# Kernel tuning notes

Measured on AMD Instinct MI355X. Metric: run time of the kernel, lower is better.

## Reference

```python
import jax, jax.numpy as jnp
import numpy as np

N_A, N_F, N_K = 512, 128, 20


def setup_inputs() -> dict:
    key = jax.random.key(0)
    ks = jax.random.split(key, 12)
    b1 = (6.0 / N_K) ** 0.5   # uniform bound for w1/w2 weights
    s_phi = 0.5 * (6.0 / N_F) ** 0.5
    inp = {
        "x": jax.random.normal(ks[0], (1, N_A, N_F), jnp.float32),
        "e": jax.random.uniform(ks[1], (1, N_A, N_A - 1, N_K), jnp.float32),
        "mask": (jax.random.uniform(ks[2], (1, N_A, N_A - 1, 1)) > 0.1).astype(jnp.float32),
        "loop_mask": ~jnp.eye(N_A, dtype=bool)[None],  # (1, n_a, n_a), False on diagonal
        "w1_w": jax.random.uniform(ks[3], (N_F, N_K), jnp.float32, -b1, b1),
        "w1_b": jnp.zeros((N_F,), jnp.float32),
        "w2_w": jax.random.uniform(ks[4], (N_F, N_K), jnp.float32, -b1, b1),
        "w2_b": jnp.zeros((N_F,), jnp.float32),
        "phi_w": s_phi * jax.random.normal(ks[5], (N_F, N_F), jnp.float32),
        "phi_b": jnp.zeros((N_F,), jnp.float32),
        "o_w": 0.05 * jax.random.normal(ks[6], (3 * N_F, 2 * N_F), jnp.float32),
        "o_b": jnp.zeros((3 * N_F,), jnp.float32),
    }
    return inp


def reference(x, e, mask, loop_mask, w1_w, w1_b, w2_w, w2_b, phi_w, phi_b, o_w, o_b):
    silu = jax.nn.silu
    # filter-generating networks on RBF expansion e: (1, n_a, n_a-1, n_k) -> (..., n_f)
    w1 = silu(jnp.einsum("bijk,fk->bijf", e, w1_w) + w1_b)
    w2 = silu(jnp.einsum("bijk,fk->bijf", e, w2_w) + w2_b)
    xp = silu(jnp.einsum("bif,gf->big", x, phi_w) + phi_b)  # (1, n_a, n_f)
    n_a = x.shape[1]
    # neighbor gather equivalent to repeat + loop_mask boolean select:
    # for row i, columns are all j != i, in order.
    j = jnp.arange(n_a - 1)[None, :]
    i = jnp.arange(n_a)[:, None]
    idx = j + (j >= i).astype(j.dtype)          # (n_a, n_a-1)
    x_nbs = xp[0][idx][None]                     # (1, n_a, n_a-1, n_f)
    v1 = xp[:, :, None, :] * w1 * mask
    v2 = x_nbs * w2 * mask
    v = (jnp.einsum("bijf,gf->bijg", jnp.concatenate([v1, v2], axis=-1), o_w) + o_b) * mask
    s1, s2, s3 = jnp.split(v, 3, axis=-1)
    return (s1, s2, s3)
```

## Files before the change

kernel.cpp:

```cpp
#include <hip/hip_runtime.h>

#define NA   512
#define NJ   511
#define NF   128
#define NK   20
#define NPAIR (NA * NJ)
#define NG   384
#define KDIM 256
#define BM   32
#define TPB  192

__global__ void xp_kernel(const float* __restrict__ x,
                          const float* __restrict__ phi_w,
                          const float* __restrict__ phi_b,
                          float* __restrict__ xp) {
    __shared__ float xs[NF];
    const int i = blockIdx.x;
    const int g = threadIdx.x;
    xs[g] = x[i * NF + g];
    __syncthreads();
    float acc = phi_b[g];
    const float* wr = phi_w + g * NF;
    #pragma unroll 8
    for (int f = 0; f < NF; ++f) acc = fmaf(xs[f], wr[f], acc);
    const float s = acc / (1.0f + __expf(-acc));
    xp[i * NF + g] = s;
}

__global__ void tr_kernel(const float* __restrict__ o_w, float* __restrict__ owT) {
    const int t = blockIdx.x * 256 + threadIdx.x;
    const int k = t / NG;
    const int g = t - k * NG;
    owT[t] = o_w[g * KDIM + k];
}

__global__ __launch_bounds__(TPB, 3)
void main_kernel(const float* __restrict__ e,
                 const float* __restrict__ mask,
                 const float* __restrict__ w1_w, const float* __restrict__ w1_b,
                 const float* __restrict__ w2_w, const float* __restrict__ w2_b,
                 const float* __restrict__ xp,
                 const float* __restrict__ owT,
                 const float* __restrict__ o_b,
                 float* __restrict__ out) {
    __shared__ float A[BM][KDIM + 4];
    __shared__ float es[BM * NK];
    __shared__ float mk[BM];
    __shared__ int   rowi[BM];
    __shared__ int   rowj[BM];

    const int p0 = blockIdx.x * BM;
    const int t  = threadIdx.x;

    for (int idx = t; idx < BM * NK; idx += TPB) es[idx] = e[p0 * NK + idx];
    if (t < BM) {
        const int p = p0 + t;
        const int i = p / NJ;
        const int j = p - i * NJ;
        rowi[t] = i;
        rowj[t] = j + (j >= i ? 1 : 0);
        mk[t]   = mask[p];
    }
    __syncthreads();

    for (int id = t; id < BM * KDIM; id += TPB) {
        const int m   = id >> 8;
        const int net = (id >> 7) & 1;
        const int f   = id & (NF - 1);
        const float* w  = (net ? w2_w : w1_w) + f * NK;
        const float* ev = es + m * NK;
        float acc = net ? w2_b[f] : w1_b[f];
        #pragma unroll
        for (int k = 0; k < NK; ++k) acc = fmaf(ev[k], w[k], acc);
        const float s = acc / (1.0f + __expf(-acc));
        const int row = net ? rowj[m] : rowi[m];
        A[m][net * NF + f] = s * xp[row * NF + f];
    }
    __syncthreads();

    const int tn = t % 48;
    const int tm = t / 48;
    float acc[8][8];
    #pragma unroll
    for (int u = 0; u < 8; ++u)
        #pragma unroll
        for (int v = 0; v < 8; ++v) acc[u][v] = 0.0f;

    const float* bbase = owT + tn * 8;
    #pragma unroll 2
    for (int k = 0; k < KDIM; ++k) {
        const float4 b0 = *(const float4*)(bbase + (size_t)k * NG);
        const float4 b1 = *(const float4*)(bbase + (size_t)k * NG + 4);
        float a[8];
        #pragma unroll
        for (int u = 0; u < 8; ++u) a[u] = A[tm * 8 + u][k];
        #pragma unroll
        for (int u = 0; u < 8; ++u) {
            acc[u][0] = fmaf(a[u], b0.x, acc[u][0]);
            acc[u][1] = fmaf(a[u], b0.y, acc[u][1]);
            acc[u][2] = fmaf(a[u], b0.z, acc[u][2]);
            acc[u][3] = fmaf(a[u], b0.w, acc[u][3]);
            acc[u][4] = fmaf(a[u], b1.x, acc[u][4]);
            acc[u][5] = fmaf(a[u], b1.y, acc[u][5]);
            acc[u][6] = fmaf(a[u], b1.z, acc[u][6]);
            acc[u][7] = fmaf(a[u], b1.w, acc[u][7]);
        }
    }

    const int g0  = tn * 8;
    const int seg = g0 >> 7;
    const int gl  = g0 & (NF - 1);
    float ob[8];
    #pragma unroll
    for (int v = 0; v < 8; ++v) ob[v] = o_b[g0 + v];
    const size_t SEG = (size_t)NPAIR * NF;
    #pragma unroll
    for (int u = 0; u < 8; ++u) {
        const int m = tm * 8 + u;
        const float mv = mk[m];
        float* op = out + (size_t)seg * SEG + (size_t)(p0 + m) * NF + gl;
        float4 r0, r1;
        r0.x = (acc[u][0] + ob[0]) * mv;
        r0.y = (acc[u][1] + ob[1]) * mv;
        r0.z = (acc[u][2] + ob[2]) * mv;
        r0.w = (acc[u][3] + ob[3]) * mv;
        r1.x = (acc[u][4] + ob[4]) * mv;
        r1.y = (acc[u][5] + ob[5]) * mv;
        r1.z = (acc[u][6] + ob[6]) * mv;
        r1.w = (acc[u][7] + ob[7]) * mv;
        *(float4*)(op)     = r0;
        *(float4*)(op + 4) = r1;
    }
}

extern "C" void kernel_launch(void* const* d_in, const int* in_sizes, int n_in,
                              void* d_out, int out_size, void* d_ws, size_t ws_size,
                              hipStream_t stream) {
    const float* x     = (const float*)d_in[0];
    const float* e     = (const float*)d_in[1];
    const float* mask  = (const float*)d_in[2];
    const float* w1_w  = (const float*)d_in[4];
    const float* w1_b  = (const float*)d_in[5];
    const float* w2_w  = (const float*)d_in[6];
    const float* w2_b  = (const float*)d_in[7];
    const float* phi_w = (const float*)d_in[8];
    const float* phi_b = (const float*)d_in[9];
    const float* o_w   = (const float*)d_in[10];
    const float* o_b   = (const float*)d_in[11];
    float* out = (float*)d_out;

    float* xp  = (float*)d_ws;
    float* owT = xp + NA * NF;

    xp_kernel<<<NA, NF, 0, stream>>>(x, phi_w, phi_b, xp);
    tr_kernel<<<(KDIM * NG) / 256, 256, 0, stream>>>(o_w, owT);
    main_kernel<<<NPAIR / BM, TPB, 0, stream>>>(e, mask, w1_w, w1_b, w2_w, w2_b,
                                                xp, owT, o_b, out);
}
```

Measured before the change: 1.128 ms.

## Use bf16 MFMA for output projection with pre-packed weights and swizzled LDS

Replaces the fp32 FMA register-tiled GEMM with bf16 MFMA 16x16x32 instructions. The filter/gather stage now writes the A operand into a swizzled shared-memory layout, and a pack kernel lays out o_w in the MFMA B-fragment order. Block size grows to 64 rows and 512 threads. The goal is to cut the compute-bound fp32 GEMM cost, at the price of bf16 rounding error and narrower scalar output stores.

After: 1.027 ms. 1.1x faster.

```diff
diff --git a/kernel.cpp b/kernel.cpp
--- a/kernel.cpp
+++ b/kernel.cpp
@@ -1,4 +1,5 @@
 #include <hip/hip_runtime.h>
+#include <hip/hip_bf16.h>
 
 #define NA   512
 #define NJ   511
@@ -7,8 +8,11 @@
 #define NPAIR (NA * NJ)
 #define NG   384
 #define KDIM 256
-#define BM   32
-#define TPB  192
+#define BM   64
+#define TPB  512
+
+using short8 = __attribute__((ext_vector_type(8))) short;
+using f32x4  = __attribute__((ext_vector_type(4))) float;
 
 __global__ void xp_kernel(const float* __restrict__ x,
                           const float* __restrict__ phi_w,
@@ -27,27 +31,33 @@
     xp[i * NF + g] = s;
 }
 
-__global__ void tr_kernel(const float* __restrict__ o_w, float* __restrict__ owT) {
-    const int t = blockIdx.x * 256 + threadIdx.x;
-    const int k = t / NG;
-    const int g = t - k * NG;
-    owT[t] = o_w[g * KDIM + k];
+__global__ void bpack_kernel(const float* __restrict__ o_w, ushort* __restrict__ bp) {
+    const int e = blockIdx.x * 256 + threadIdx.x;
+    const int j    = e & 7;
+    const int l    = (e >> 3) & 63;
+    const int rest = e >> 9;
+    const int nf   = rest % 24;
+    const int kb   = rest / 24;
+    const int g = nf * 16 + (l & 15);
+    const int k = kb * 32 + (l >> 4) * 8 + j;
+    __hip_bfloat16 h = __float2bfloat16(o_w[g * KDIM + k]);
+    bp[e] = *reinterpret_cast<ushort*>(&h);
 }
 
-__global__ __launch_bounds__(TPB, 3)
+__global__ __launch_bounds__(TPB, 2)
 void main_kernel(const float* __restrict__ e,
                  const float* __restrict__ mask,
                  const float* __restrict__ w1_w, const float* __restrict__ w1_b,
                  const float* __restrict__ w2_w, const float* __restrict__ w2_b,
                  const float* __restrict__ xp,
-                 const float* __restrict__ owT,
+                 const ushort* __restrict__ bp,
                  const float* __restrict__ o_b,
                  float* __restrict__ out) {
-    __shared__ float A[BM][KDIM + 4];
-    __shared__ float es[BM * NK];
-    __shared__ float mk[BM];
-    __shared__ int   rowi[BM];
-    __shared__ int   rowj[BM];
+    __shared__ short8 Ash[BM * 32];
+    __shared__ float  es[BM * NK];
+    __shared__ float  mk[BM];
+    __shared__ int    rowi[BM];
+    __shared__ int    rowj[BM];
 
     const int p0 = blockIdx.x * BM;
     const int t  = threadIdx.x;
@@ -63,73 +73,79 @@
     }
     __syncthreads();
 
-    for (int id = t; id < BM * KDIM; id += TPB) {
-        const int m   = id >> 8;
-        const int net = (id >> 7) & 1;
-        const int f   = id & (NF - 1);
-        const float* w  = (net ? w2_w : w1_w) + f * NK;
+    for (int id = t; id < BM * 32; id += TPB) {
+        const int kg  = id & 31;
+        const int m   = id >> 5;
+        const int net = kg >> 4;
+        const float* wmat = net ? w2_w : w1_w;
+        const float* wbv  = net ? w2_b : w1_b;
+        const int row = net ? rowj[m] : rowi[m];
         const float* ev = es + m * NK;
-        float acc = net ? w2_b[f] : w1_b[f];
+        const float* xr = xp + row * NF;
+        const int f0 = (kg & 15) * 8;
+        short8 pk;
         #pragma unroll
-        for (int k = 0; k < NK; ++k) acc = fmaf(ev[k], w[k], acc);
-        const float s = acc / (1.0f + __expf(-acc));
-        const int row = net ? rowj[m] : rowi[m];
-        A[m][net * NF + f] = s * xp[row * NF + f];
+        for (int j = 0; j < 8; ++j) {
+            const int f = f0 + j;
+            const float* wr = wmat + f * NK;
+            float acc = wbv[f];
+            #pragma unroll
+            for (int k = 0; k < NK; ++k) acc = fmaf(ev[k], wr[k], acc);
+            const float s   = acc / (1.0f + __expf(-acc));
+            const float val = s * xr[f];
+            __hip_bfloat16 h = __float2bfloat16(val);
+            pk[j] = *reinterpret_cast<const short*>(&h);
+        }
+        Ash[m * 32 + (kg ^ (m & 7))] = pk;
     }
     __syncthreads();
 
-    const int tn = t % 48;
-    const int tm = t / 48;
-    float acc[8][8];
+    const int wave = t >> 6, lane = t & 63;
+    const int wm = wave & 1, wn = wave >> 1;
+    const int lr = lane & 15;
+    const int lk = lane >> 4;
+
+    const f32x4 zero = {0.0f, 0.0f, 0.0f, 0.0f};
+    f32x4 acc[2][6];
     #pragma unroll
-    for (int u = 0; u < 8; ++u)
+    for (int mf = 0; mf < 2; ++mf)
         #pragma unroll
-        for (int v = 0; v < 8; ++v) acc[u][v] = 0.0f;
+        for (int nf = 0; nf < 6; ++nf) acc[mf][nf] = zero;
 
-    const float* bbase = owT + tn * 8;
-    #pragma unroll 2
-    for (int k = 0; k < KDIM; ++k) {
-        const float4 b0 = *(const float4*)(bbase + (size_t)k * NG);
-        const float4 b1 = *(const float4*)(bbase + (size_t)k * NG + 4);
-        float a[8];
+    const short8* bpv = (const short8*)bp;
+    const int r0 = wm * 32 + lr;
+    const int r1 = r0 + 16;
+    #pragma unroll
+    for (int ks = 0; ks < 8; ++ks) {
+        const int kg = ks * 4 + lk;
+        const short8 a0 = Ash[r0 * 32 + (kg ^ (r0 & 7))];
+        const short8 a1 = Ash[r1 * 32 + (kg ^ (r1 & 7))];
         #pragma unroll
-        for (int u = 0; u < 8; ++u) a[u] = A[tm * 8 + u][k];
-        #pragma unroll
-        for (int u = 0; u < 8; ++u) {
-            acc[u][0] = fmaf(a[u], b0.x, acc[u][0]);
-            acc[u][1] = fmaf(a[u], b0.y, acc[u][1]);
-            acc[u][2] = fmaf(a[u], b0.z, acc[u][2]);
-            acc[u][3] = fmaf(a[u], b0.w, acc[u][3]);
-            acc[u][4] = fmaf(a[u], b1.x, acc[u][4]);
-            acc[u][5] = fmaf(a[u], b1.y, acc[u][5]);
-            acc[u][6] = fmaf(a[u], b1.z, acc[u][6]);
-            acc[u][7] = fmaf(a[u], b1.w, acc[u][7]);
+        for (int nf = 0; nf < 6; ++nf) {
+            const short8 b = bpv[((ks * 24 + wn * 6 + nf) * 64) + lane];
+            acc[0][nf] = __builtin_amdgcn_mfma_f32_16x16x32_bf16(a0, b, acc[0][nf], 0, 0, 0);
+            acc[1][nf] = __builtin_amdgcn_mfma_f32_16x16x32_bf16(a1, b, acc[1][nf], 0, 0, 0);
         }
     }
 
-    const int g0  = tn * 8;
-    const int seg = g0 >> 7;
-    const int gl  = g0 & (NF - 1);
-    float ob[8];
-    #pragma unroll
-    for (int v = 0; v < 8; ++v) ob[v] = o_b[g0 + v];
     const size_t SEG = (size_t)NPAIR * NF;
     #pragma unroll
-    for (int u = 0; u < 8; ++u) {
-        const int m = tm * 8 + u;
-        const float mv = mk[m];
-        float* op = out + (size_t)seg * SEG + (size_t)(p0 + m) * NF + gl;
-        float4 r0, r1;
-        r0.x = (acc[u][0] + ob[0]) * mv;
-        r0.y = (acc[u][1] + ob[1]) * mv;
-        r0.z = (acc[u][2] + ob[2]) * mv;
-        r0.w = (acc[u][3] + ob[3]) * mv;
-        r1.x = (acc[u][4] + ob[4]) * mv;
-        r1.y = (acc[u][5] + ob[5]) * mv;
-        r1.z = (acc[u][6] + ob[6]) * mv;
-        r1.w = (acc[u][7] + ob[7]) * mv;
-        *(float4*)(op)     = r0;
-        *(float4*)(op + 4) = r1;
+    for (int nf = 0; nf < 6; ++nf) {
+        const int g   = wn * 96 + nf * 16 + lr;
+        const int seg = g >> 7;
+        const int gl  = g & (NF - 1);
+        const float obv = o_b[g];
+        float* obase = out + (size_t)seg * SEG + gl;
+        #pragma unroll
+        for (int mf = 0; mf < 2; ++mf) {
+            const int mloc = wm * 32 + mf * 16 + lk * 4;
+            #pragma unroll
+            for (int r = 0; r < 4; ++r) {
+                const int m = mloc + r;
+                const float v = (acc[mf][nf][r] + obv) * mk[m];
+                obase[(size_t)(p0 + m) * NF] = v;
+            }
+        }
     }
 }
 
@@ -149,11 +165,11 @@
     const float* o_b   = (const float*)d_in[11];
     float* out = (float*)d_out;
 
-    float* xp  = (float*)d_ws;
-    float* owT = xp + NA * NF;
+    float*  xp = (float*)d_ws;
+    ushort* bpk = (ushort*)((char*)d_ws + NA * NF * 4);
 
     xp_kernel<<<NA, NF, 0, stream>>>(x, phi_w, phi_b, xp);
-    tr_kernel<<<(KDIM * NG) / 256, 256, 0, stream>>>(o_w, owT);
+    bpack_kernel<<<(8 * 24 * 64 * 8) / 256, 256, 0, stream>>>(o_w, bpk);
     main_kernel<<<NPAIR / BM, TPB, 0, stream>>>(e, mask, w1_w, w1_b, w2_w, w2_b,
-                                                xp, owT, o_b, out);
+                                                xp, bpk, o_b, out);
 }
```
